# Optimization experiments

Measured on AMD Instinct MI355X. Metric: run time of the kernel, lower is better.

The kernel has to match this reference:

```python
import jax, jax.numpy as jnp
import numpy as np

B, S, D = 8, 1024, 768
H = 12
DH = D // H  # 64
SCALE = 1.0 / (D ** 0.5)  # module scales by full embedding_dim, not head_dim


def setup_inputs() -> dict:
    key = jax.random.key(0)
    ks = jax.random.split(key, 7)
    std = 1.0 / np.sqrt(D)
    return {
        "x": jax.random.normal(ks[0], (B, S, D), dtype=jnp.float32),
        "Wq": jax.random.uniform(ks[1], (D, D), jnp.float32, -std, std),
        "bq": jax.random.uniform(ks[2], (D,), jnp.float32, -std, std),
        "Wk": jax.random.uniform(ks[3], (D, D), jnp.float32, -std, std),
        "bk": jax.random.uniform(ks[4], (D,), jnp.float32, -std, std),
        "Wv": jax.random.uniform(ks[5], (D, D), jnp.float32, -std, std),
        "bv": jax.random.uniform(ks[6], (D,), jnp.float32, -std, std),
    }


def reference(x, Wq, bq, Wk, bk, Wv, bv):
    b, s, d = x.shape
    # projections; torch.chunk(dim=-1) == reshape last dim to [H, DH]
    q = (x @ Wq + bq).reshape(b, s, H, DH)
    k = (x @ Wk + bk).reshape(b, s, H, DH)
    v = (x @ Wv + bv).reshape(b, s, H, DH)
    # per-head scores [b, h, s, s], scaled by sqrt(embedding_dim) per source
    scores = jnp.einsum("bqhd,bkhd->bhqk", q, k) * SCALE
    attn = jax.nn.softmax(scores, axis=-1)
    out = jnp.einsum("bhqk,bkhd->bqhd", attn, v)
    # concat heads back along last dim (order matches chunk order)
    return out.reshape(b, s, d)
```

## Files before the change

### kernel.cpp

```cpp
#include <hip/hip_runtime.h>
#include <cstdint>
#include <cstddef>

typedef unsigned short u16;
typedef unsigned int u32;
typedef unsigned char u8;

using bfx8 = __attribute__((ext_vector_type(8))) __bf16;
using floatx4 = __attribute__((ext_vector_type(4))) float;

static constexpr int kS = 1024;
static constexpr int kD = 768;
static constexpr int kH = 12;
static constexpr int kDH = 64;
#define SCALE 0.036084391824351614f

__device__ __forceinline__ u16 f2bf(float f) {
    u32 u = __float_as_uint(f);
    return (u16)((u + 0x7fffu + ((u >> 16) & 1u)) >> 16);
}

__device__ __forceinline__ void gld16(const void* g, void* l) {
    __builtin_amdgcn_global_load_lds(
        (__attribute__((address_space(1))) const u32*)g,
        (__attribute__((address_space(3))) u32*)l, 16, 0, 0);
}

__global__ __launch_bounds__(256) void cvt_x(const float* __restrict__ x, u16* __restrict__ xb) {
    int i = (blockIdx.x * 256 + threadIdx.x) * 4;
    float4 v = *(const float4*)(x + i);
    u32 lo = (u32)f2bf(v.x) | ((u32)f2bf(v.y) << 16);
    u32 hi = (u32)f2bf(v.z) | ((u32)f2bf(v.w) << 16);
    *(uint2*)(xb + i) = make_uint2(lo, hi);
}

__global__ __launch_bounds__(256) void cvt_w(const float* __restrict__ w0, const float* __restrict__ w1,
                                             const float* __restrict__ w2, u16* __restrict__ wt) {
    __shared__ float t[32][33];
    const float* W = blockIdx.z == 0 ? w0 : (blockIdx.z == 1 ? w1 : w2);
    u16* dst = wt + (size_t)blockIdx.z * kD * kD;
    int k0 = blockIdx.x * 32, n0 = blockIdx.y * 32;
    int tx = threadIdx.x, ty = threadIdx.y;
#pragma unroll
    for (int j = 0; j < 4; j++)
        t[ty + j * 8][tx] = W[(size_t)(k0 + ty + j * 8) * kD + n0 + tx];
    __syncthreads();
#pragma unroll
    for (int j = 0; j < 4; j++)
        dst[(size_t)(n0 + ty + j * 8) * kD + k0 + tx] = f2bf(t[tx][ty + j * 8]);
}

__global__ __launch_bounds__(256) void proj(const u16* __restrict__ xb, const u16* __restrict__ wt,
                                            const float* __restrict__ bq, const float* __restrict__ bk,
                                            const float* __restrict__ bvp,
                                            u16* __restrict__ qb, u16* __restrict__ kb, u16* __restrict__ vt) {
    __shared__ u16 As[128 * 64];
    __shared__ u16 Bs[128 * 64];
    int m0 = blockIdx.x * 128;
    int n0g = blockIdx.y * 128;
    int t = threadIdx.x;
    int w = t >> 6, lane = t & 63, lanelo = lane & 15, quad = lane >> 4;
    int wm = (w & 1) * 64, wn = (w >> 1) * 64;
    int rloc8 = lane >> 3, p8 = lane & 7;
    int chw = p8 ^ rloc8;
    const u16* Brow = wt + (size_t)n0g * kD;
    floatx4 acc[4][4] = {};
    for (int ks = 0; ks < kD; ks += 64) {
        __syncthreads();
#pragma unroll
        for (int i = 0; i < 4; i++) {
            int j = w * 4 + i;
            int r = 8 * j + rloc8;
            gld16(xb + (size_t)(m0 + r) * kD + ks + chw * 8, &As[j * 512]);
            gld16(Brow + (size_t)r * kD + ks + chw * 8, &Bs[j * 512]);
        }
        __syncthreads();
#pragma unroll
        for (int kk = 0; kk < 2; kk++) {
            int co = ((kk * 4 + quad) ^ (lanelo & 7)) * 8;
            bfx8 a[4], b[4];
#pragma unroll
            for (int mf = 0; mf < 4; mf++)
                a[mf] = *(const bfx8*)&As[(wm + mf * 16 + lanelo) * 64 + co];
#pragma unroll
            for (int nf = 0; nf < 4; nf++)
                b[nf] = *(const bfx8*)&Bs[(wn + nf * 16 + lanelo) * 64 + co];
#pragma unroll
            for (int mf = 0; mf < 4; mf++)
#pragma unroll
                for (int nf = 0; nf < 4; nf++)
                    acc[mf][nf] = __builtin_amdgcn_mfma_f32_16x16x32_bf16(a[mf], b[nf], acc[mf][nf], 0, 0, 0);
        }
    }
    int zz = blockIdx.y / 6;
    int nl0 = (blockIdx.y - zz * 6) * 128;
    const float* bias = zz == 0 ? bq : (zz == 1 ? bk : bvp);
    float mul = zz == 0 ? SCALE : 1.0f;
#pragma unroll
    for (int nf = 0; nf < 4; nf++) {
        int nl = nl0 + wn + nf * 16 + lanelo;
        float bb = bias[nl];
#pragma unroll
        for (int mf = 0; mf < 4; mf++) {
            if (zz < 2) {
                u16* dst = zz == 0 ? qb : kb;
#pragma unroll
                for (int reg = 0; reg < 4; reg++) {
                    int m = m0 + wm + mf * 16 + quad * 4 + reg;
                    dst[(size_t)m * kD + nl] = f2bf((acc[mf][nf][reg] + bb) * mul);
                }
            } else {
                int m = m0 + wm + mf * 16 + quad * 4;
                int bi = m >> 10, s = m & 1023;
                int hh = nl >> 6, dh = nl & 63;
                u32 lo = (u32)f2bf(acc[mf][nf][0] + bb) | ((u32)f2bf(acc[mf][nf][1] + bb) << 16);
                u32 hi = (u32)f2bf(acc[mf][nf][2] + bb) | ((u32)f2bf(acc[mf][nf][3] + bb) << 16);
                *(uint2*)&vt[(((size_t)bi * kH + hh) * kDH + dh) * kS + s] = make_uint2(lo, hi);
            }
        }
    }
}

__global__ __launch_bounds__(256, 4) void attn(const u16* __restrict__ qb, const u16* __restrict__ kb,
                                               const u16* __restrict__ vt, float* __restrict__ out) {
    __shared__ u16 Qs[64 * 64];
    __shared__ u16 KPs[128 * 64];
    __shared__ u16 Vs[64 * 128];
    int q0 = blockIdx.x * 64;
    int bh = blockIdx.y;
    int b = bh / kH, h = bh % kH;
    int t = threadIdx.x, w = t >> 6, lane = t & 63, lanelo = lane & 15, quad = lane >> 4;
    int rloc8 = lane >> 3, p8 = lane & 7;
    int chw8 = p8 ^ rloc8;

#pragma unroll
    for (int i = 0; i < 2; i++) {
        int j = 2 * w + i;
        int r = 8 * j + rloc8;
        gld16(qb + (size_t)(b * kS + q0 + r) * kD + h * kDH + chw8 * 8, &Qs[j * 512]);
    }

    float rsum = 0.f;
    floatx4 oacc[4] = {};

    for (int kt = 0; kt < 8; kt++) {
        int kk0 = kt * 128;
        __syncthreads();
#pragma unroll
        for (int i = 0; i < 4; i++) {
            int j = 4 * w + i;
            int r = 8 * j + rloc8;
            gld16(kb + (size_t)(b * kS + kk0 + r) * kD + h * kDH + chw8 * 8, &KPs[j * 512]);
        }
#pragma unroll
        for (int i = 0; i < 4; i++) {
            int j = 4 * w + i;
            int r = 4 * j + quad;
            int ch = lanelo ^ (r & 15);
            gld16(vt + (((size_t)b * kH + h) * kDH + r) * kS + kk0 + ch * 8, &Vs[j * 512]);
        }
        __syncthreads();

        floatx4 sacc[8] = {};
#pragma unroll
        for (int kk = 0; kk < 2; kk++) {
            int co = ((kk * 4 + quad) ^ (lanelo & 7)) * 8;
            bfx8 bq_ = *(const bfx8*)&Qs[(w * 16 + lanelo) * 64 + co];
#pragma unroll
            for (int mf = 0; mf < 8; mf++) {
                bfx8 ak = *(const bfx8*)&KPs[(mf * 16 + lanelo) * 64 + co];
                sacc[mf] = __builtin_amdgcn_mfma_f32_16x16x32_bf16(ak, bq_, sacc[mf], 0, 0, 0);
            }
        }
        __syncthreads();

#pragma unroll
        for (int mf = 0; mf < 8; mf++) {
            float p0 = __expf(sacc[mf][0]);
            float p1 = __expf(sacc[mf][1]);
            float p2 = __expf(sacc[mf][2]);
            float p3 = __expf(sacc[mf][3]);
            rsum += (p0 + p1) + (p2 + p3);
            u32 lo = (u32)f2bf(p0) | ((u32)f2bf(p1) << 16);
            u32 hi = (u32)f2bf(p2) | ((u32)f2bf(p3) << 16);
            int pch = (2 * mf + (quad >> 1)) ^ lanelo;
            *(uint2*)((u8*)KPs + (w * 16 + lanelo) * 256 + pch * 16 + (quad & 1) * 8) = make_uint2(lo, hi);
        }

#pragma unroll
        for (int ks2 = 0; ks2 < 4; ks2++) {
            bfx8 ap = *(const bfx8*)((const u8*)KPs + (w * 16 + lanelo) * 256 + ((4 * ks2 + quad) ^ lanelo) * 16);
#pragma unroll
            for (int nf = 0; nf < 4; nf++) {
                bfx8 bv_ = *(const bfx8*)((const u8*)Vs + (nf * 16 + lanelo) * 256 + ((4 * ks2 + quad) ^ lanelo) * 16);
                oacc[nf] = __builtin_amdgcn_mfma_f32_16x16x32_bf16(ap, bv_, oacc[nf], 0, 0, 0);
            }
        }
    }

    rsum += __shfl_xor(rsum, 16, 64);
    rsum += __shfl_xor(rsum, 32, 64);
    float linv[4];
#pragma unroll
    for (int reg = 0; reg < 4; reg++)
        linv[reg] = 1.0f / __shfl(rsum, quad * 4 + reg, 64);
#pragma unroll
    for (int nf = 0; nf < 4; nf++)
#pragma unroll
        for (int reg = 0; reg < 4; reg++)
            out[(size_t)(b * kS + q0 + w * 16 + quad * 4 + reg) * kD + h * kDH + nf * 16 + lanelo] =
                oacc[nf][reg] * linv[reg];
}

extern "C" void kernel_launch(void* const* d_in, const int* in_sizes, int n_in,
                              void* d_out, int out_size, void* d_ws, size_t ws_size,
                              hipStream_t stream) {
    const float* x  = (const float*)d_in[0];
    const float* Wq = (const float*)d_in[1];
    const float* bq = (const float*)d_in[2];
    const float* Wk = (const float*)d_in[3];
    const float* bk = (const float*)d_in[4];
    const float* Wv = (const float*)d_in[5];
    const float* bv = (const float*)d_in[6];
    float* out = (float*)d_out;

    u16* ws = (u16*)d_ws;
    u16* xb = ws;
    u16* wt = xb + 6291456;
    u16* qb = wt + 1769472;
    u16* kb = qb + 6291456;
    u16* vt = kb + 6291456;

    cvt_x<<<dim3(6144), dim3(256), 0, stream>>>(x, xb);
    cvt_w<<<dim3(24, 24, 3), dim3(32, 8), 0, stream>>>(Wq, Wk, Wv, wt);
    proj<<<dim3(64, 18), dim3(256), 0, stream>>>(xb, wt, bq, bk, bv, qb, kb, vt);
    attn<<<dim3(16, 96), dim3(256), 0, stream>>>(qb, kb, vt, out);
}
```

Baseline: 191.5 us.

## Switch projection and attention MFMAs to 32x32x16 tiles and repartition attention waves

Both the projection GEMM and the attention kernel replace 16x16x32 bf16 MFMAs with 32x32x16 MFMAs. Each wave now owns larger output fragments, which cuts LDS fragment reads per FLOP. In attention, the four waves are split as 2 query halves by 2 key halves. Q fragments are held in registers instead of LDS, and the two partial row sums are merged through shared memory at the end. The cost is higher accumulator register pressure and an extra barrier per key tile before the PV step.

```diff
diff --git a/kernel.cpp b/kernel.cpp
--- a/kernel.cpp
+++ b/kernel.cpp
@@ -7,7 +7,7 @@
 typedef unsigned char u8;
 
 using bfx8 = __attribute__((ext_vector_type(8))) __bf16;
-using floatx4 = __attribute__((ext_vector_type(4))) float;
+using floatx16 = __attribute__((ext_vector_type(16))) float;
 
 static constexpr int kS = 1024;
 static constexpr int kD = 768;
@@ -59,12 +59,14 @@
     int m0 = blockIdx.x * 128;
     int n0g = blockIdx.y * 128;
     int t = threadIdx.x;
-    int w = t >> 6, lane = t & 63, lanelo = lane & 15, quad = lane >> 4;
+    int w = t >> 6, lane = t & 63;
+    int l31 = lane & 31, hi = lane >> 5;
     int wm = (w & 1) * 64, wn = (w >> 1) * 64;
     int rloc8 = lane >> 3, p8 = lane & 7;
     int chw = p8 ^ rloc8;
     const u16* Brow = wt + (size_t)n0g * kD;
-    floatx4 acc[4][4] = {};
+    int swz = l31 & 7;
+    floatx16 acc[2][2] = {};
     for (int ks = 0; ks < kD; ks += 64) {
         __syncthreads();
 #pragma unroll
@@ -76,20 +78,19 @@
         }
         __syncthreads();
 #pragma unroll
-        for (int kk = 0; kk < 2; kk++) {
-            int co = ((kk * 4 + quad) ^ (lanelo & 7)) * 8;
-            bfx8 a[4], b[4];
-#pragma unroll
-            for (int mf = 0; mf < 4; mf++)
-                a[mf] = *(const bfx8*)&As[(wm + mf * 16 + lanelo) * 64 + co];
-#pragma unroll
-            for (int nf = 0; nf < 4; nf++)
-                b[nf] = *(const bfx8*)&Bs[(wn + nf * 16 + lanelo) * 64 + co];
-#pragma unroll
-            for (int mf = 0; mf < 4; mf++)
-#pragma unroll
-                for (int nf = 0; nf < 4; nf++)
-                    acc[mf][nf] = __builtin_amdgcn_mfma_f32_16x16x32_bf16(a[mf], b[nf], acc[mf][nf], 0, 0, 0);
+        for (int s = 0; s < 4; s++) {
+            int tc = ((s * 2 + hi) ^ swz) * 8;
+            bfx8 a[2], bf[2];
+#pragma unroll
+            for (int i = 0; i < 2; i++) {
+                a[i] = *(const bfx8*)&As[(wm + i * 32 + l31) * 64 + tc];
+                bf[i] = *(const bfx8*)&Bs[(wn + i * 32 + l31) * 64 + tc];
+            }
+#pragma unroll
+            for (int i = 0; i < 2; i++)
+#pragma unroll
+                for (int j = 0; j < 2; j++)
+                    acc[i][j] = __builtin_amdgcn_mfma_f32_32x32x16_bf16(a[i], bf[j], acc[i][j], 0, 0, 0);
         }
     }
     int zz = blockIdx.y / 6;
@@ -97,25 +98,29 @@
     const float* bias = zz == 0 ? bq : (zz == 1 ? bk : bvp);
     float mul = zz == 0 ? SCALE : 1.0f;
 #pragma unroll
-    for (int nf = 0; nf < 4; nf++) {
-        int nl = nl0 + wn + nf * 16 + lanelo;
+    for (int j = 0; j < 2; j++) {
+        int nl = nl0 + wn + j * 32 + l31;
         float bb = bias[nl];
 #pragma unroll
-        for (int mf = 0; mf < 4; mf++) {
+        for (int i = 0; i < 2; i++) {
+            int mbase = m0 + wm + i * 32 + 4 * hi;
             if (zz < 2) {
                 u16* dst = zz == 0 ? qb : kb;
 #pragma unroll
-                for (int reg = 0; reg < 4; reg++) {
-                    int m = m0 + wm + mf * 16 + quad * 4 + reg;
-                    dst[(size_t)m * kD + nl] = f2bf((acc[mf][nf][reg] + bb) * mul);
+                for (int reg = 0; reg < 16; reg++) {
+                    int m = mbase + (reg & 3) + 8 * (reg >> 2);
+                    dst[(size_t)m * kD + nl] = f2bf((acc[i][j][reg] + bb) * mul);
                 }
             } else {
-                int m = m0 + wm + mf * 16 + quad * 4;
-                int bi = m >> 10, s = m & 1023;
                 int hh = nl >> 6, dh = nl & 63;
-                u32 lo = (u32)f2bf(acc[mf][nf][0] + bb) | ((u32)f2bf(acc[mf][nf][1] + bb) << 16);
-                u32 hi = (u32)f2bf(acc[mf][nf][2] + bb) | ((u32)f2bf(acc[mf][nf][3] + bb) << 16);
-                *(uint2*)&vt[(((size_t)bi * kH + hh) * kDH + dh) * kS + s] = make_uint2(lo, hi);
+#pragma unroll
+                for (int g = 0; g < 4; g++) {
+                    int m = mbase + 8 * g;
+                    int bi = m >> 10, s = m & 1023;
+                    u32 lo = (u32)f2bf(acc[i][j][4 * g + 0] + bb) | ((u32)f2bf(acc[i][j][4 * g + 1] + bb) << 16);
+                    u32 h2 = (u32)f2bf(acc[i][j][4 * g + 2] + bb) | ((u32)f2bf(acc[i][j][4 * g + 3] + bb) << 16);
+                    *(uint2*)&vt[(((size_t)bi * kH + hh) * kDH + dh) * kS + s] = make_uint2(lo, h2);
+                }
             }
         }
     }
@@ -123,93 +128,98 @@
 
 __global__ __launch_bounds__(256, 4) void attn(const u16* __restrict__ qb, const u16* __restrict__ kb,
                                                const u16* __restrict__ vt, float* __restrict__ out) {
-    __shared__ u16 Qs[64 * 64];
     __shared__ u16 KPs[128 * 64];
     __shared__ u16 Vs[64 * 128];
+    __shared__ float Lw[2][64];
     int q0 = blockIdx.x * 64;
     int bh = blockIdx.y;
     int b = bh / kH, h = bh % kH;
-    int t = threadIdx.x, w = t >> 6, lane = t & 63, lanelo = lane & 15, quad = lane >> 4;
-    int rloc8 = lane >> 3, p8 = lane & 7;
-    int chw8 = p8 ^ rloc8;
-
-#pragma unroll
-    for (int i = 0; i < 2; i++) {
-        int j = 2 * w + i;
-        int r = 8 * j + rloc8;
-        gld16(qb + (size_t)(b * kS + q0 + r) * kD + h * kDH + chw8 * 8, &Qs[j * 512]);
-    }
-
+    int t = threadIdx.x, w = t >> 6, lane = t & 63;
+    int l31 = lane & 31, hi = lane >> 5;
+    int qh = w & 1, kh = w >> 1;
+
+    bfx8 qf[4];
+    {
+        const u16* qrow = qb + (size_t)(b * kS + q0 + qh * 32 + l31) * kD + h * kDH + hi * 8;
+#pragma unroll
+        for (int f = 0; f < 4; f++) qf[f] = *(const bfx8*)(qrow + f * 16);
+    }
+
+    int qrl = qh * 32 + l31;
+    int pswz = qrl & 15;
     float rsum = 0.f;
-    floatx4 oacc[4] = {};
+    floatx16 oacc = {};
 
     for (int kt = 0; kt < 8; kt++) {
         int kk0 = kt * 128;
         __syncthreads();
 #pragma unroll
         for (int i = 0; i < 4; i++) {
-            int j = 4 * w + i;
-            int r = 8 * j + rloc8;
-            gld16(kb + (size_t)(b * kS + kk0 + r) * kD + h * kDH + chw8 * 8, &KPs[j * 512]);
+            int jj = 4 * w + i;
+            int r = 8 * jj + (lane >> 3);
+            int c = (lane & 7) ^ ((lane >> 3) & 7);
+            gld16(kb + (size_t)(b * kS + kk0 + r) * kD + h * kDH + c * 8, &KPs[jj * 512]);
         }
 #pragma unroll
         for (int i = 0; i < 4; i++) {
-            int j = 4 * w + i;
-            int r = 4 * j + quad;
-            int ch = lanelo ^ (r & 15);
-            gld16(vt + (((size_t)b * kH + h) * kDH + r) * kS + kk0 + ch * 8, &Vs[j * 512]);
-        }
-        __syncthreads();
-
-        floatx4 sacc[8] = {};
-#pragma unroll
-        for (int kk = 0; kk < 2; kk++) {
-            int co = ((kk * 4 + quad) ^ (lanelo & 7)) * 8;
-            bfx8 bq_ = *(const bfx8*)&Qs[(w * 16 + lanelo) * 64 + co];
-#pragma unroll
-            for (int mf = 0; mf < 8; mf++) {
-                bfx8 ak = *(const bfx8*)&KPs[(mf * 16 + lanelo) * 64 + co];
-                sacc[mf] = __builtin_amdgcn_mfma_f32_16x16x32_bf16(ak, bq_, sacc[mf], 0, 0, 0);
-            }
-        }
-        __syncthreads();
-
-#pragma unroll
-        for (int mf = 0; mf < 8; mf++) {
-            float p0 = __expf(sacc[mf][0]);
-            float p1 = __expf(sacc[mf][1]);
-            float p2 = __expf(sacc[mf][2]);
-            float p3 = __expf(sacc[mf][3]);
-            rsum += (p0 + p1) + (p2 + p3);
-            u32 lo = (u32)f2bf(p0) | ((u32)f2bf(p1) << 16);
-            u32 hi = (u32)f2bf(p2) | ((u32)f2bf(p3) << 16);
-            int pch = (2 * mf + (quad >> 1)) ^ lanelo;
-            *(uint2*)((u8*)KPs + (w * 16 + lanelo) * 256 + pch * 16 + (quad & 1) * 8) = make_uint2(lo, hi);
-        }
-
-#pragma unroll
-        for (int ks2 = 0; ks2 < 4; ks2++) {
-            bfx8 ap = *(const bfx8*)((const u8*)KPs + (w * 16 + lanelo) * 256 + ((4 * ks2 + quad) ^ lanelo) * 16);
-#pragma unroll
-            for (int nf = 0; nf < 4; nf++) {
-                bfx8 bv_ = *(const bfx8*)((const u8*)Vs + (nf * 16 + lanelo) * 256 + ((4 * ks2 + quad) ^ lanelo) * 16);
-                oacc[nf] = __builtin_amdgcn_mfma_f32_16x16x32_bf16(ap, bv_, oacc[nf], 0, 0, 0);
-            }
-        }
-    }
-
-    rsum += __shfl_xor(rsum, 16, 64);
+            int jj = 4 * w + i;
+            int r = 4 * jj + (lane >> 4);
+            int c = (lane & 15) ^ (r & 15);
+            gld16(vt + (((size_t)b * kH + h) * kDH + r) * kS + kk0 + c * 8, &Vs[jj * 512]);
+        }
+        __syncthreads();
+
+        floatx16 sacc[2] = {};
+#pragma unroll
+        for (int s = 0; s < 4; s++) {
+#pragma unroll
+            for (int fm = 0; fm < 2; fm++) {
+                int row = kh * 64 + fm * 32 + l31;
+                int tc = ((s * 2 + hi) ^ (l31 & 7)) * 8;
+                bfx8 ak = *(const bfx8*)&KPs[row * 64 + tc];
+                sacc[fm] = __builtin_amdgcn_mfma_f32_32x32x16_bf16(ak, qf[s], sacc[fm], 0, 0, 0);
+            }
+        }
+        __syncthreads();
+
+        u8* prow = (u8*)KPs + qrl * 256;
+#pragma unroll
+        for (int fm = 0; fm < 2; fm++) {
+#pragma unroll
+            for (int g = 0; g < 4; g++) {
+                float p0 = __expf(sacc[fm][4 * g + 0]);
+                float p1 = __expf(sacc[fm][4 * g + 1]);
+                float p2 = __expf(sacc[fm][4 * g + 2]);
+                float p3 = __expf(sacc[fm][4 * g + 3]);
+                rsum += (p0 + p1) + (p2 + p3);
+                u32 lo = (u32)f2bf(p0) | ((u32)f2bf(p1) << 16);
+                u32 h2 = (u32)f2bf(p2) | ((u32)f2bf(p3) << 16);
+                int c16 = kh * 8 + fm * 4 + g;
+                *(uint2*)(prow + ((c16 ^ pswz) * 2 + hi) * 8) = make_uint2(lo, h2);
+            }
+        }
+        __syncthreads();
+
+#pragma unroll
+        for (int s = 0; s < 8; s++) {
+            bfx8 ap = *(const bfx8*)(prow + ((s * 2 + hi) ^ pswz) * 16);
+            bfx8 bv = *(const bfx8*)((const u8*)Vs + (kh * 32 + l31) * 256 + (((s * 2 + hi) ^ (l31 & 15)) * 16));
+            oacc = __builtin_amdgcn_mfma_f32_32x32x16_bf16(ap, bv, oacc, 0, 0, 0);
+        }
+    }
+
     rsum += __shfl_xor(rsum, 32, 64);
-    float linv[4];
-#pragma unroll
-    for (int reg = 0; reg < 4; reg++)
-        linv[reg] = 1.0f / __shfl(rsum, quad * 4 + reg, 64);
-#pragma unroll
-    for (int nf = 0; nf < 4; nf++)
-#pragma unroll
-        for (int reg = 0; reg < 4; reg++)
-            out[(size_t)(b * kS + q0 + w * 16 + quad * 4 + reg) * kD + h * kDH + nf * 16 + lanelo] =
-                oacc[nf][reg] * linv[reg];
+    if (lane < 32) Lw[kh][qh * 32 + lane] = rsum;
+    __syncthreads();
+#pragma unroll
+    for (int g = 0; g < 4; g++) {
+#pragma unroll
+        for (int r2 = 0; r2 < 4; r2++) {
+            int qloc = qh * 32 + r2 + 8 * g + 4 * hi;
+            float linv = 1.0f / (Lw[0][qloc] + Lw[1][qloc]);
+            out[(size_t)(b * kS + q0 + qloc) * kD + h * kDH + kh * 32 + l31] = oacc[4 * g + r2] * linv;
+        }
+    }
 }
 
 extern "C" void kernel_launch(void* const* d_in, const int* in_sizes, int n_in,
```

After: 184.7 us. 1.04x faster.
